# Optimization experiments

Hardware: AMD Instinct MI355X
Metric: run time of the kernel (lower is better)

The kernel has to match this reference:

```python
import jax, jax.numpy as jnp
import numpy as np

B, S, D = 64, 2048, 64

def setup_inputs() -> dict:
    key = jax.random.key(0)
    kq, kk, kv = jax.random.split(key, 3)
    queries = jax.random.normal(kq, (B, S, D), dtype=jnp.float32)
    keys = jax.random.normal(kk, (B, S, D), dtype=jnp.float32)
    values = jax.random.normal(kv, (B, S, D), dtype=jnp.float32)
    return {"queries": queries, "keys": keys, "values": values}

def reference(queries, keys, values):
    # scores: [B, Sq, Sk] = Q @ K^T / sqrt(d)
    d = queries.shape[-1]
    scale = 1.0 / jnp.sqrt(jnp.asarray(d, dtype=queries.dtype))
    scores = jnp.einsum('bqd,bkd->bqk', queries, keys) * scale
    attn = jax.nn.softmax(scores, axis=-1)
    # dropout is identity in eval/reference mode
    return jnp.einsum('bqk,bkd->bqd', attn, values)
```

## Files before the change

kernel.cpp:

```cpp
#include <hip/hip_runtime.h>


typedef short bf16x8 __attribute__((ext_vector_type(8)));
typedef float f32x4 __attribute__((ext_vector_type(4)));

#define SQK 0.18033688011112042f

__device__ __forceinline__ short f2bf(float x) {
  unsigned u = __float_as_uint(x);
  u = (u + 0x7fffu + ((u >> 16) & 1u)) >> 16;
  return (short)u;
}

__device__ __forceinline__ unsigned pk2(float lo, float hi) {
  unsigned r;
  asm("v_cvt_pk_bf16_f32 %0, %1, %2" : "=v"(r) : "v"(lo), "v"(hi));
  return r;
}

__global__ __launch_bounds__(512) void DotProductAttention_44573170598739_kernel(
    const float* __restrict__ Q, const float* __restrict__ K,
    const float* __restrict__ V, float* __restrict__ O) {
  constexpr int S = 2048, D = 64;
  const int b   = blockIdx.x;
  const int q0  = blockIdx.y * 256;
  const int tid = threadIdx.x;
  const int w    = tid >> 6;
  const int lane = tid & 63;
  const int qh   = lane >> 4;
  const int r    = lane & 15;

  __shared__ __align__(16) short ksh[64 * 72];
  __shared__ __align__(16) short vsh[64 * 72];
  __shared__ __align__(16) short psh[8][32 * 72];

  bf16x8 qf[2][2];
#pragma unroll
  for (int s = 0; s < 2; ++s)
#pragma unroll
    for (int c = 0; c < 2; ++c) {
      const float* qp = Q + ((size_t)b * S + q0 + w * 32 + s * 16 + r) * D + c * 32 + qh * 8;
      float4 x = ((const float4*)qp)[0];
      float4 y = ((const float4*)qp)[1];
      bf16x8 f;
      f[0] = f2bf(x.x * SQK); f[1] = f2bf(x.y * SQK);
      f[2] = f2bf(x.z * SQK); f[3] = f2bf(x.w * SQK);
      f[4] = f2bf(y.x * SQK); f[5] = f2bf(y.y * SQK);
      f[6] = f2bf(y.z * SQK); f[7] = f2bf(y.w * SQK);
      qf[s][c] = f;
    }

  bf16x8 onesf;
#pragma unroll
  for (int i = 0; i < 8; ++i) onesf[i] = (short)0x3F80;

  f32x4 oacc[2][4] = {};
  f32x4 sacc[2] = {};
  const f32x4 zf = {};

  const float* Kb = K + (size_t)b * S * D;
  const float* Vb = V + (size_t)b * S * D;

  float4 kx[2];
  float  vv[8];
#pragma unroll
  for (int i = 0; i < 2; ++i)
    kx[i] = ((const float4*)Kb)[tid + 512 * i];
#pragma unroll
  for (int j = 0; j < 8; ++j)
    vv[j] = Vb[(w * 8 + j) * D + lane];

  for (int kt = 0; kt < S; kt += 64) {
#pragma unroll
    for (int i = 0; i < 2; ++i) {
      int f = 4 * tid + 2048 * i;
      int row = f >> 6, col = f & 63;
      uint2 pk = { pk2(kx[i].x, kx[i].y), pk2(kx[i].z, kx[i].w) };
      *(uint2*)&ksh[row * 72 + col] = pk;
    }
#pragma unroll
    for (int jj = 0; jj < 2; ++jj) {
      uint2 pk = { pk2(vv[4 * jj + 0], vv[4 * jj + 1]),
                   pk2(vv[4 * jj + 2], vv[4 * jj + 3]) };
      *(uint2*)&vsh[lane * 72 + w * 8 + 4 * jj] = pk;
    }
    __syncthreads();

    bf16x8 kf[4][2], vf[4][2];
#pragma unroll
    for (int t = 0; t < 4; ++t)
#pragma unroll
      for (int c = 0; c < 2; ++c) {
        kf[t][c] = *(const bf16x8*)&ksh[(t * 16 + r) * 72 + c * 32 + qh * 8];
        vf[t][c] = *(const bf16x8*)&vsh[(t * 16 + r) * 72 + c * 32 + qh * 8];
      }

    {
      const int kt2 = (kt + 64 < S) ? kt + 64 : 0;
      const float* Kg2 = Kb + (size_t)kt2 * D;
      const float* Vg2 = Vb + (size_t)kt2 * D;
#pragma unroll
      for (int i = 0; i < 2; ++i)
        kx[i] = ((const float4*)Kg2)[tid + 512 * i];
#pragma unroll
      for (int j = 0; j < 8; ++j)
        vv[j] = Vg2[(w * 8 + j) * D + lane];
    }

#pragma unroll
    for (int s = 0; s < 2; ++s) {
      f32x4 sc[4];
#pragma unroll
      for (int t = 0; t < 4; ++t) {
        f32x4 z = __builtin_amdgcn_mfma_f32_16x16x32_bf16(kf[t][0], qf[s][0], zf, 0, 0, 0);
        z = __builtin_amdgcn_mfma_f32_16x16x32_bf16(kf[t][1], qf[s][1], z, 0, 0, 0);
        sc[t] = z;
      }
#pragma unroll
      for (int t = 0; t < 4; ++t)
#pragma unroll
        for (int g = 0; g < 4; ++g)
          sc[t][g] = __builtin_amdgcn_exp2f(sc[t][g]);
#pragma unroll
      for (int t = 0; t < 4; ++t) {
        uint2 pk = { pk2(sc[t][0], sc[t][1]), pk2(sc[t][2], sc[t][3]) };
        *(uint2*)&psh[w][(s * 16 + r) * 72 + t * 16 + 4 * qh] = pk;
      }
    }

    __asm__ volatile("s_waitcnt lgkmcnt(0)" ::: "memory");
#pragma unroll
    for (int s = 0; s < 2; ++s)
#pragma unroll
      for (int c = 0; c < 2; ++c) {
        bf16x8 pf = *(const bf16x8*)&psh[w][(s * 16 + r) * 72 + c * 32 + qh * 8];
        sacc[s] = __builtin_amdgcn_mfma_f32_16x16x32_bf16(pf, onesf, sacc[s], 0, 0, 0);
#pragma unroll
        for (int dt = 0; dt < 4; ++dt)
          oacc[s][dt] = __builtin_amdgcn_mfma_f32_16x16x32_bf16(pf, vf[dt][c], oacc[s][dt], 0, 0, 0);
      }
    __syncthreads();
  }

#pragma unroll
  for (int s = 0; s < 2; ++s)
#pragma unroll
    for (int g = 0; g < 4; ++g) {
      float inv = 1.0f / sacc[s][g];
      int q = q0 + w * 32 + s * 16 + 4 * qh + g;
      float* op = O + ((size_t)b * S + q) * D + r;
#pragma unroll
      for (int dt = 0; dt < 4; ++dt)
        op[dt * 16] = oacc[s][dt][g] * inv;
    }
}

extern "C" void kernel_launch(void* const* d_in, const int* in_sizes, int n_in,
                              void* d_out, int out_size, void* d_ws, size_t ws_size,
                              hipStream_t stream) {
  (void)in_sizes; (void)n_in; (void)out_size; (void)d_ws; (void)ws_size;
  const float* Q = (const float*)d_in[0];
  const float* K = (const float*)d_in[1];
  const float* V = (const float*)d_in[2];
  float* O = (float*)d_out;
  dim3 grid(64, 2048 / 256, 1);
  dim3 block(512, 1, 1);
  hipLaunchKernelGGL(DotProductAttention_44573170598739_kernel,
                     grid, block, 0, stream, Q, K, V, O);
}
```

Baseline: 210.3 us.

## Switch to 32x32x16 MFMA and keep P in registers without LDS round-trip

Replaces the 16x16x32 MFMA tiling with 32x32x16 MFMAs, arranged so the S^T accumulator layout maps directly onto the A-operand layout for the P·V product. This removes the per-warp P staging buffer in shared memory along with its wait. The row sum is now accumulated in scalar registers with a final cross-lane shuffle, replacing the ones-vector MFMA. The V shared-memory write layout is permuted to match the new operand order. In exchange the code relies on a carefully permuted V layout and a new output index mapping that must both be exactly right.

```diff
diff --git a/kernel.cpp b/kernel.cpp
--- a/kernel.cpp
+++ b/kernel.cpp
@@ -2,7 +2,7 @@
 
 
 typedef short bf16x8 __attribute__((ext_vector_type(8)));
-typedef float f32x4 __attribute__((ext_vector_type(4)));
+typedef float f32x16 __attribute__((ext_vector_type(16)));
 
 #define SQK 0.18033688011112042f
 
@@ -27,36 +27,29 @@
   const int tid = threadIdx.x;
   const int w    = tid >> 6;
   const int lane = tid & 63;
-  const int qh   = lane >> 4;
-  const int r    = lane & 15;
+  const int hi   = lane >> 5;
+  const int r32  = lane & 31;
 
   __shared__ __align__(16) short ksh[64 * 72];
   __shared__ __align__(16) short vsh[64 * 72];
-  __shared__ __align__(16) short psh[8][32 * 72];
 
-  bf16x8 qf[2][2];
+  bf16x8 qf[4];
 #pragma unroll
-  for (int s = 0; s < 2; ++s)
-#pragma unroll
-    for (int c = 0; c < 2; ++c) {
-      const float* qp = Q + ((size_t)b * S + q0 + w * 32 + s * 16 + r) * D + c * 32 + qh * 8;
-      float4 x = ((const float4*)qp)[0];
-      float4 y = ((const float4*)qp)[1];
-      bf16x8 f;
-      f[0] = f2bf(x.x * SQK); f[1] = f2bf(x.y * SQK);
-      f[2] = f2bf(x.z * SQK); f[3] = f2bf(x.w * SQK);
-      f[4] = f2bf(y.x * SQK); f[5] = f2bf(y.y * SQK);
-      f[6] = f2bf(y.z * SQK); f[7] = f2bf(y.w * SQK);
-      qf[s][c] = f;
-    }
+  for (int dd = 0; dd < 4; ++dd) {
+    const float* qp = Q + ((size_t)b * S + q0 + w * 32 + r32) * D + dd * 16 + hi * 8;
+    float4 x = ((const float4*)qp)[0];
+    float4 y = ((const float4*)qp)[1];
+    bf16x8 f;
+    f[0] = f2bf(x.x * SQK); f[1] = f2bf(x.y * SQK);
+    f[2] = f2bf(x.z * SQK); f[3] = f2bf(x.w * SQK);
+    f[4] = f2bf(y.x * SQK); f[5] = f2bf(y.y * SQK);
+    f[6] = f2bf(y.z * SQK); f[7] = f2bf(y.w * SQK);
+    qf[dd] = f;
+  }
 
-  bf16x8 onesf;
-#pragma unroll
-  for (int i = 0; i < 8; ++i) onesf[i] = (short)0x3F80;
-
-  f32x4 oacc[2][4] = {};
-  f32x4 sacc[2] = {};
-  const f32x4 zf = {};
+  f32x16 oacc[2] = {};
+  float rs = 0.f;
+  const f32x16 z16 = {};
 
   const float* Kb = K + (size_t)b * S * D;
   const float* Vb = V + (size_t)b * S * D;
@@ -70,6 +63,8 @@
   for (int j = 0; j < 8; ++j)
     vv[j] = Vb[(w * 8 + j) * D + lane];
 
+  const int vcb = 16 * (w >> 1) + 4 * (w & 1);
+
   for (int kt = 0; kt < S; kt += 64) {
 #pragma unroll
     for (int i = 0; i < 2; ++i) {
@@ -78,81 +73,74 @@
       uint2 pk = { pk2(kx[i].x, kx[i].y), pk2(kx[i].z, kx[i].w) };
       *(uint2*)&ksh[row * 72 + col] = pk;
     }
-#pragma unroll
-    for (int jj = 0; jj < 2; ++jj) {
-      uint2 pk = { pk2(vv[4 * jj + 0], vv[4 * jj + 1]),
-                   pk2(vv[4 * jj + 2], vv[4 * jj + 3]) };
-      *(uint2*)&vsh[lane * 72 + w * 8 + 4 * jj] = pk;
+    {
+      uint2 plo = { pk2(vv[0], vv[1]), pk2(vv[2], vv[3]) };
+      uint2 phi = { pk2(vv[4], vv[5]), pk2(vv[6], vv[7]) };
+      *(uint2*)&vsh[lane * 72 + vcb]     = plo;
+      *(uint2*)&vsh[lane * 72 + vcb + 8] = phi;
     }
     __syncthreads();
 
-    bf16x8 kf[4][2], vf[4][2];
 #pragma unroll
-    for (int t = 0; t < 4; ++t)
+    for (int t = 0; t < 2; ++t) {
+      bf16x8 kf[4];
 #pragma unroll
-      for (int c = 0; c < 2; ++c) {
-        kf[t][c] = *(const bf16x8*)&ksh[(t * 16 + r) * 72 + c * 32 + qh * 8];
-        vf[t][c] = *(const bf16x8*)&vsh[(t * 16 + r) * 72 + c * 32 + qh * 8];
+      for (int dd = 0; dd < 4; ++dd)
+        kf[dd] = *(const bf16x8*)&ksh[(t * 32 + r32) * 72 + dd * 16 + hi * 8];
+
+      if (t == 0) {
+        const int kt2 = (kt + 64 < S) ? kt + 64 : 0;
+        const float* Kg2 = Kb + (size_t)kt2 * D;
+        const float* Vg2 = Vb + (size_t)kt2 * D;
+#pragma unroll
+        for (int i = 0; i < 2; ++i)
+          kx[i] = ((const float4*)Kg2)[tid + 512 * i];
+#pragma unroll
+        for (int j = 0; j < 8; ++j)
+          vv[j] = Vg2[(w * 8 + j) * D + lane];
       }
 
-    {
-      const int kt2 = (kt + 64 < S) ? kt + 64 : 0;
-      const float* Kg2 = Kb + (size_t)kt2 * D;
-      const float* Vg2 = Vb + (size_t)kt2 * D;
-#pragma unroll
-      for (int i = 0; i < 2; ++i)
-        kx[i] = ((const float4*)Kg2)[tid + 512 * i];
-#pragma unroll
-      for (int j = 0; j < 8; ++j)
-        vv[j] = Vg2[(w * 8 + j) * D + lane];
-    }
+      f32x16 z = __builtin_amdgcn_mfma_f32_32x32x16_bf16(kf[0], qf[0], z16, 0, 0, 0);
+      z = __builtin_amdgcn_mfma_f32_32x32x16_bf16(kf[1], qf[1], z, 0, 0, 0);
+      z = __builtin_amdgcn_mfma_f32_32x32x16_bf16(kf[2], qf[2], z, 0, 0, 0);
+      z = __builtin_amdgcn_mfma_f32_32x32x16_bf16(kf[3], qf[3], z, 0, 0, 0);
 
 #pragma unroll
-    for (int s = 0; s < 2; ++s) {
-      f32x4 sc[4];
-#pragma unroll
-      for (int t = 0; t < 4; ++t) {
-        f32x4 z = __builtin_amdgcn_mfma_f32_16x16x32_bf16(kf[t][0], qf[s][0], zf, 0, 0, 0);
-        z = __builtin_amdgcn_mfma_f32_16x16x32_bf16(kf[t][1], qf[s][1], z, 0, 0, 0);
-        sc[t] = z;
-      }
-#pragma unroll
-      for (int t = 0; t < 4; ++t)
-#pragma unroll
-        for (int g = 0; g < 4; ++g)
-          sc[t][g] = __builtin_amdgcn_exp2f(sc[t][g]);
-#pragma unroll
-      for (int t = 0; t < 4; ++t) {
-        uint2 pk = { pk2(sc[t][0], sc[t][1]), pk2(sc[t][2], sc[t][3]) };
-        *(uint2*)&psh[w][(s * 16 + r) * 72 + t * 16 + 4 * qh] = pk;
+      for (int h = 0; h < 2; ++h) {
+        float e0 = __builtin_amdgcn_exp2f(z[8 * h + 0]);
+        float e1 = __builtin_amdgcn_exp2f(z[8 * h + 1]);
+        float e2 = __builtin_amdgcn_exp2f(z[8 * h + 2]);
+        float e3 = __builtin_amdgcn_exp2f(z[8 * h + 3]);
+        float e4 = __builtin_amdgcn_exp2f(z[8 * h + 4]);
+        float e5 = __builtin_amdgcn_exp2f(z[8 * h + 5]);
+        float e6 = __builtin_amdgcn_exp2f(z[8 * h + 6]);
+        float e7 = __builtin_amdgcn_exp2f(z[8 * h + 7]);
+        rs += ((e0 + e1) + (e2 + e3)) + ((e4 + e5) + (e6 + e7));
+        union { bf16x8 v; unsigned u[4]; } pu;
+        pu.u[0] = pk2(e0, e1); pu.u[1] = pk2(e2, e3);
+        pu.u[2] = pk2(e4, e5); pu.u[3] = pk2(e6, e7);
+
+        const int cb = t * 32 + h * 16 + hi * 8;
+        bf16x8 vf0 = *(const bf16x8*)&vsh[(r32) * 72 + cb];
+        bf16x8 vf1 = *(const bf16x8*)&vsh[(32 + r32) * 72 + cb];
+
+        oacc[0] = __builtin_amdgcn_mfma_f32_32x32x16_bf16(pu.v, vf0, oacc[0], 0, 0, 0);
+        oacc[1] = __builtin_amdgcn_mfma_f32_32x32x16_bf16(pu.v, vf1, oacc[1], 0, 0, 0);
       }
     }
-
-    __asm__ volatile("s_waitcnt lgkmcnt(0)" ::: "memory");
-#pragma unroll
-    for (int s = 0; s < 2; ++s)
-#pragma unroll
-      for (int c = 0; c < 2; ++c) {
-        bf16x8 pf = *(const bf16x8*)&psh[w][(s * 16 + r) * 72 + c * 32 + qh * 8];
-        sacc[s] = __builtin_amdgcn_mfma_f32_16x16x32_bf16(pf, onesf, sacc[s], 0, 0, 0);
-#pragma unroll
-        for (int dt = 0; dt < 4; ++dt)
-          oacc[s][dt] = __builtin_amdgcn_mfma_f32_16x16x32_bf16(pf, vf[dt][c], oacc[s][dt], 0, 0, 0);
-      }
     __syncthreads();
   }
 
+  float tot = rs + __shfl_xor(rs, 32);
 #pragma unroll
-  for (int s = 0; s < 2; ++s)
-#pragma unroll
-    for (int g = 0; g < 4; ++g) {
-      float inv = 1.0f / sacc[s][g];
-      int q = q0 + w * 32 + s * 16 + 4 * qh + g;
-      float* op = O + ((size_t)b * S + q) * D + r;
-#pragma unroll
-      for (int dt = 0; dt < 4; ++dt)
-        op[dt * 16] = oacc[s][dt][g] * inv;
-    }
+  for (int g = 0; g < 16; ++g) {
+    int rq = (g & 3) + 8 * (g >> 2) + 4 * hi;
+    float inv = 1.0f / __shfl(tot, rq);
+    int q = q0 + w * 32 + rq;
+    float* op = O + ((size_t)b * S + q) * D + r32;
+    op[0]  = oacc[0][g] * inv;
+    op[32] = oacc[1][g] * inv;
+  }
 }
 
 extern "C" void kernel_launch(void* const* d_in, const int* in_sizes, int n_in,
```

Result: faster. 202.4 us (-3.7%).
